# Performance work log

Measured on AMD Instinct MI355X. Metric: run time of the kernel, lower is better.

## Reference

```python
import jax, jax.numpy as jnp
import numpy as np

N, K, D = 16384, 16, 16
TWO_PI = 2.0 * np.pi


def setup_inputs() -> dict:
    key = jax.random.key(0)
    k1, k2, k3, k4 = jax.random.split(key, 4)
    X = jax.random.normal(k1, (N, D), dtype=jnp.float32)
    mu = jax.random.normal(k2, (K, D), dtype=jnp.float32)
    L = jax.random.normal(k3, (K, D, D), dtype=jnp.float32)
    weights = jax.random.uniform(k4, (K,), dtype=jnp.float32)
    return {"X": X, "mu": mu, "L": L, "weights": weights, "it": 0}


def reference(X, mu, L, weights, it):
    # Covariance matrices A_k = tril(L_k) @ tril(L_k)^T + I  -> [K, D, D]
    Tl = jnp.tril(L)
    A = jnp.einsum('kab,kcb->kac', Tl, Tl) + jnp.eye(D, dtype=L.dtype)
    Sigma = jnp.linalg.inv(A)                                  # [K, D, D]

    # Gaussian product for all pairs (i, j):
    #   S_ij = inv(Sigma_i + Sigma_j), m_ij = S_ij (Sigma_i mu_i + Sigma_j mu_j)
    Ssum = Sigma[:, None] + Sigma[None, :]                     # [K, K, D, D]
    S = jnp.linalg.inv(Ssum)                                   # [K, K, D, D]
    rhs = jnp.einsum('kab,kb->ka', Sigma, mu)                  # Sigma_k mu_k
    m = jnp.einsum('ijab,ijb->ija', S, rhs[:, None] + rhs[None, :])  # [K, K, D]

    # Normalizer of the product Gaussian: z_ij = ((2pi)^D det(S_ij))^(-1/2)
    z = 1.0 / jnp.sqrt((TWO_PI ** D) * jnp.linalg.det(S))      # [K, K]
    P = jnp.linalg.inv(S)                                      # precision, [K, K, D, D]

    # Pair coefficient _product_z(i, j) (uses A as covariance here, as in source)
    Asum = A[:, None] + A[None, :]                             # [K, K, D, D]
    dmu = mu[:, None] - mu[None, :]                            # [K, K, D]
    q_mu = jnp.einsum('ijd,ijde,ije->ij', dmu, jnp.linalg.inv(Asum), dmu)
    pz = jnp.exp(-0.5 * q_mu) / jnp.sqrt(jnp.linalg.det(TWO_PI * Asum))

    # Mahalanobis distance of every sample to every pair mean: [N, K, K]
    diff = X[:, None, None, :] - m[None]                       # [N, K, K, D]
    quad = jnp.einsum('nijd,ijde,nije->nij', diff, P, diff)

    coef = pz * z * (weights[:, None] * weights[None, :])      # [K, K]
    pdf = jnp.einsum('ij,nij->n', coef, jnp.exp(-0.5 * quad))  # [N]
    return jnp.mean(jnp.log(pdf))
```

## Files before the change

### kernel.cpp

```cpp
#include <hip/hip_runtime.h>
#include <math.h>

#define NTOT 16384
#define KK 16
#define DD 16
#define NPAIR 136

#define NPREP 9

#define WS_RHS   0
#define WS_WP    1024
#define WS_LCS   9792
#define WS_PART  10336
#define WS_END   18528

#define LN2PI 1.8378770664093454836f

#define SROW 17
#define SMAT (SROW * DD)

__device__ __forceinline__ float chol16_rl(float* Mr, int r, float* dinvv) {
  float ld = 0.0f;
  #pragma unroll
  for (int c = 0; c < DD; c++) {
    float d2 = __shfl(Mr[c], c, 16);
    ld += __logf(d2);
    float dinv = rsqrtf(d2);
    dinvv[c] = dinv;
    float v = Mr[c] * dinv;
    Mr[c] = v;
    #pragma unroll
    for (int c2 = c + 1; c2 < DD; c2++)
      Mr[c2] = fmaf(-v, __shfl(v, c2, 16), Mr[c2]);
  }
  return ld;
}

__device__ __forceinline__ float solve16(const float* G, int r,
                                         const float* dinvv, float b) {
  float acc = b, qq = 0.0f;
  #pragma unroll
  for (int m = 0; m < DD; m++) {
    float ym = __shfl(acc, m, 16) * dinvv[m];
    qq = fmaf(ym, ym, qq);
    if (r > m) acc = fmaf(-G[m], ym, acc);
  }
  return qq;
}

__global__ __launch_bounds__(256) void gm_prep(const float* __restrict__ mu,
                                               const float* __restrict__ L,
                                               const float* __restrict__ wts,
                                               char* __restrict__ wsb) {
  __shared__ float sSig[KK * SMAT];
  __shared__ float sA[KK * SMAT];
  __shared__ float sR[256];

  const int tid = threadIdx.x;
  const int k = tid >> 4;
  const int r = tid & 15;

  const float* Lk = L + k * DD * DD;
  float Lx[DD];
  #pragma unroll
  for (int b = 0; b < DD; b++) Lx[b] = (b <= r) ? Lk[r * DD + b] : 0.0f;

  float Ar[DD];
  #pragma unroll
  for (int c = 0; c < DD; c++) {
    float s = (r == c) ? 1.0f : 0.0f;
    #pragma unroll
    for (int b = 0; b <= c; b++)
      s = fmaf(Lx[b], __shfl(Lx[b], c, 16), s);
    Ar[c] = s;
    sA[k * SMAT + r * SROW + c] = s;
  }

  float dinvv[DD];
  chol16_rl(Ar, r, dinvv);

  float Wc[DD];
  {
    float acc[DD];
    #pragma unroll
    for (int m = 0; m < DD; m++) acc[m] = (r == m) ? 1.0f : 0.0f;
    #pragma unroll
    for (int m = 0; m < DD; m++) {
      float w = acc[m] * dinvv[m];
      Wc[m] = w;
      #pragma unroll
      for (int rr = m + 1; rr < DD; rr++)
        acc[rr] = fmaf(-__shfl(Ar[m], rr, 16), w, acc[rr]);
    }
  }
  if (blockIdx.x == 0) {
    float* Wout = (float*)(wsb + WS_WP) + k * 137;
    #pragma unroll
    for (int rr = 0; rr < DD; rr++)
      if (rr >= r) Wout[rr * (rr + 1) / 2 + r] = Wc[rr];
  }

  float Sig[DD];
  #pragma unroll
  for (int b = 0; b < DD; b++) {
    float s = 0.0f;
    #pragma unroll
    for (int rr = 0; rr < DD; rr++)
      s = fmaf(Wc[rr], __shfl(Wc[rr], b, 16), s);
    Sig[b] = s;
    sSig[k * SMAT + r * SROW + b] = s;
  }

  {
    float muv = mu[k * DD + r];
    float s = 0.0f;
    #pragma unroll
    for (int b = 0; b < DD; b++)
      s = fmaf(Sig[b], __shfl(muv, b, 16), s);
    sR[k * DD + r] = s;
    if (blockIdx.x == 0) ((float*)(wsb + WS_RHS))[k * DD + r] = s;
  }
  __syncthreads();

  const int p = blockIdx.x * 16 + k;
  if (p >= NPAIR) return;
  int i = 0, rem = p;
  while (rem >= (KK - i)) { rem -= (KK - i); i++; }
  const int j = i + rem;

  float Mr[DD];
  float dv[DD];

  #pragma unroll
  for (int c = 0; c < DD; c++)
    Mr[c] = sSig[i * SMAT + r * SROW + c] + sSig[j * SMAT + r * SROW + c];
  float ldS = chol16_rl(Mr, r, dv);
  float cq = solve16(Mr, r, dv, sR[i * DD + r] + sR[j * DD + r]);

  #pragma unroll
  for (int c = 0; c < DD; c++)
    Mr[c] = sA[i * SMAT + r * SROW + c] + sA[j * SMAT + r * SROW + c];
  float ldA = chol16_rl(Mr, r, dv);
  float q = solve16(Mr, r, dv, mu[i * DD + r] - mu[j * DD + r]);

  if (r == 0) {
    float lC = -0.5f * q - 0.5f * ldA + 0.5f * ldS - (float)DD * LN2PI
               + __logf(wts[i]) + __logf(wts[j]) - 0.5f * cq;
    if (i < j) lC += 0.69314718056f;
    ((float*)(wsb + WS_LCS))[p] = lC;
  }
}

__global__ __launch_bounds__(256) void gm_main(const float* __restrict__ X,
                                               char* __restrict__ wsb) {
  __shared__ float sW[KK * 137];
  __shared__ float sR[KK * 17];
  __shared__ float sLC[NPAIR];
  __shared__ unsigned char sIJ[NPAIR];
  __shared__ float sX[256];
  __shared__ float sE[16 * 17];
  __shared__ double sD[16];

  const int tid = threadIdx.x;
  const int s = tid >> 4;
  const int r = tid & 15;

  {
    const float* Wp = (const float*)(wsb + WS_WP);
    for (int idx = tid; idx < KK * 137; idx += 256) sW[idx] = Wp[idx];
    const float* Rf = (const float*)(wsb + WS_RHS);
    sR[s * 17 + r] = Rf[tid];
    const float* lc = (const float*)(wsb + WS_LCS);
    if (tid < NPAIR) {
      sLC[tid] = lc[tid];
      int i = 0, rem = tid;
      while (rem >= (KK - i)) { rem -= (KK - i); i++; }
      sIJ[tid] = (unsigned char)((i << 4) | (i + rem));
    }
    if (tid < 64)
      ((float4*)sX)[tid] = ((const float4*)(X + (size_t)blockIdx.x * 256))[tid];
  }
  __syncthreads();

  float x[DD];
  {
    float4 b0 = ((const float4*)sX)[s * 4 + 0];
    float4 b1 = ((const float4*)sX)[s * 4 + 1];
    float4 b2 = ((const float4*)sX)[s * 4 + 2];
    float4 b3 = ((const float4*)sX)[s * 4 + 3];
    x[0]=b0.x; x[1]=b0.y; x[2]=b0.z; x[3]=b0.w;
    x[4]=b1.x; x[5]=b1.y; x[6]=b1.z; x[7]=b1.w;
    x[8]=b2.x; x[9]=b2.y; x[10]=b2.z; x[11]=b2.w;
    x[12]=b3.x; x[13]=b3.y; x[14]=b3.z; x[15]=b3.w;
  }

  {
    const float* Wk = &sW[r * 137];
    float g = 0.0f;
    #pragma unroll
    for (int rr = 0; rr < DD; rr++) {
      float y = 0.0f;
      #pragma unroll
      for (int c = 0; c <= rr; c++) y = fmaf(Wk[rr * (rr + 1) / 2 + c], x[c], y);
      g = fmaf(y, y, g);
    }
    float h = 0.0f;
    #pragma unroll
    for (int d = 0; d < DD; d++) h = fmaf(sR[r * 17 + d], x[d], h);
    sE[s * 17 + r] = fmaf(-0.5f, g, h);
  }
  __syncthreads();

  float val[9];
  float T = -3.0e38f;
  #pragma unroll
  for (int t = 0; t < 9; t++) {
    int p = t * 16 + r;
    if (t < 8 || r < 8) {
      int ij = sIJ[p];
      val[t] = sLC[p] + sE[s * 17 + (ij >> 4)] + sE[s * 17 + (ij & 15)];
    } else {
      val[t] = -3.0e38f;
    }
    T = fmaxf(T, val[t]);
  }
  #pragma unroll
  for (int w = 1; w < 16; w <<= 1) T = fmaxf(T, __shfl_xor(T, w, 16));

  float sum = 0.0f;
  #pragma unroll
  for (int t = 0; t < 9; t++) sum += __expf(val[t] - T);
  #pragma unroll
  for (int w = 1; w < 16; w <<= 1) sum += __shfl_xor(sum, w, 16);

  if (r == 0) sD[s] = (double)(T + __logf(sum));
  __syncthreads();
  if (tid == 0) {
    double acc = 0.0;
    #pragma unroll
    for (int m = 0; m < 16; m++) acc += sD[m];
    ((double*)(wsb + WS_PART))[blockIdx.x] = acc;
  }
}

__global__ __launch_bounds__(256) void gm_fin(const double* __restrict__ part,
                                              float* __restrict__ out) {
  int t = threadIdx.x;
  double v = part[t] + part[t + 256] + part[t + 512] + part[t + 768];
  #pragma unroll
  for (int off = 32; off > 0; off >>= 1) v += __shfl_down(v, off);
  __shared__ double r4[4];
  if ((t & 63) == 0) r4[t >> 6] = v;
  __syncthreads();
  if (t == 0) out[0] = (float)((r4[0] + r4[1] + r4[2] + r4[3]) * (1.0 / 16384.0));
}

extern "C" void kernel_launch(void* const* d_in, const int* in_sizes, int n_in,
                              void* d_out, int out_size, void* d_ws, size_t ws_size,
                              hipStream_t stream) {
  const float* X   = (const float*)d_in[0];
  const float* mu  = (const float*)d_in[1];
  const float* L   = (const float*)d_in[2];
  const float* wts = (const float*)d_in[3];
  char* wsb = (char*)d_ws;
  if (ws_size < WS_END) return;

  hipLaunchKernelGGL(gm_prep, dim3(NPREP), dim3(256), 0, stream, mu, L, wts, wsb);
  hipLaunchKernelGGL(gm_main, dim3(NTOT / 16), dim3(256), 0, stream, X, wsb);
  hipLaunchKernelGGL(gm_fin,  dim3(1), dim3(256), 0, stream,
                     (const double*)(wsb + WS_PART), (float*)d_out);
}
```

Measured before the change: 32.09 us.

## Fuse final reduction into main kernel via fixed-point atomics and interleave dual Cholesky

The separate final-reduction kernel is removed. Each main block now adds its partial log-sum to a global 64-bit fixed-point accumulator with an atomic, and the last block to finish, found through an atomic counter, writes the mean. A memset clears the accumulator and counter before the prep kernel. Separately, the two pairwise Cholesky factorisations and solves in the prep kernel are interleaved to expose more instruction-level parallelism. The gain is one fewer kernel launch and a shorter prep critical path, at the cost of an extra memset launch and fixed-point rounding of the partial sums.

Result: slower. 57.65 us (+79.6%).

```diff
diff --git a/kernel.cpp b/kernel.cpp
--- a/kernel.cpp
+++ b/kernel.cpp
@@ -7,17 +7,62 @@
 #define NPAIR 136
 
 #define NPREP 9
+#define NMAIN 1024
 
 #define WS_RHS   0
 #define WS_WP    1024
 #define WS_LCS   9792
-#define WS_PART  10336
-#define WS_END   18528
+#define WS_ACC   10336
+#define WS_CNT   10344
+#define WS_END   10352
 
 #define LN2PI 1.8378770664093454836f
+#define FXSCALE 268435456.0
 
 #define SROW 17
 #define SMAT (SROW * DD)
+
+__device__ __forceinline__ void chol16_rl2(float* Ms, float* Ma, int r,
+                                           float* dinvS, float* dinvA,
+                                           float& ldS, float& ldA) {
+  float ls = 0.0f, la = 0.0f;
+  #pragma unroll
+  for (int c = 0; c < DD; c++) {
+    float d2s = __shfl(Ms[c], c, 16);
+    float d2a = __shfl(Ma[c], c, 16);
+    ls += __logf(d2s);
+    la += __logf(d2a);
+    float dis = rsqrtf(d2s), dia = rsqrtf(d2a);
+    dinvS[c] = dis; dinvA[c] = dia;
+    float vs = Ms[c] * dis, va = Ma[c] * dia;
+    Ms[c] = vs; Ma[c] = va;
+    #pragma unroll
+    for (int c2 = c + 1; c2 < DD; c2++) {
+      Ms[c2] = fmaf(-vs, __shfl(vs, c2, 16), Ms[c2]);
+      Ma[c2] = fmaf(-va, __shfl(va, c2, 16), Ma[c2]);
+    }
+  }
+  ldS = ls; ldA = la;
+}
+
+__device__ __forceinline__ void solve16_2(const float* Gs, const float* Ga, int r,
+                                          const float* dinvS, const float* dinvA,
+                                          float bs, float ba,
+                                          float& qs, float& qa) {
+  float accS = bs, accA = ba, s = 0.0f, a = 0.0f;
+  #pragma unroll
+  for (int m = 0; m < DD; m++) {
+    float ys = __shfl(accS, m, 16) * dinvS[m];
+    float ya = __shfl(accA, m, 16) * dinvA[m];
+    s = fmaf(ys, ys, s);
+    a = fmaf(ya, ya, a);
+    if (r > m) {
+      accS = fmaf(-Gs[m], ys, accS);
+      accA = fmaf(-Ga[m], ya, accA);
+    }
+  }
+  qs = s; qa = a;
+}
 
 __device__ __forceinline__ float chol16_rl(float* Mr, int r, float* dinvv) {
   float ld = 0.0f;
@@ -36,22 +81,10 @@
   return ld;
 }
 
-__device__ __forceinline__ float solve16(const float* G, int r,
-                                         const float* dinvv, float b) {
-  float acc = b, qq = 0.0f;
-  #pragma unroll
-  for (int m = 0; m < DD; m++) {
-    float ym = __shfl(acc, m, 16) * dinvv[m];
-    qq = fmaf(ym, ym, qq);
-    if (r > m) acc = fmaf(-G[m], ym, acc);
-  }
-  return qq;
-}
-
-__global__ __launch_bounds__(256) void gm_prep(const float* __restrict__ mu,
-                                               const float* __restrict__ L,
-                                               const float* __restrict__ wts,
-                                               char* __restrict__ wsb) {
+__global__ __launch_bounds__(256, 1) void gm_prep(const float* __restrict__ mu,
+                                                  const float* __restrict__ L,
+                                                  const float* __restrict__ wts,
+                                                  char* __restrict__ wsb) {
   __shared__ float sSig[KK * SMAT];
   __shared__ float sA[KK * SMAT];
   __shared__ float sR[256];
@@ -128,20 +161,19 @@
   while (rem >= (KK - i)) { rem -= (KK - i); i++; }
   const int j = i + rem;
 
-  float Mr[DD];
-  float dv[DD];
-
-  #pragma unroll
-  for (int c = 0; c < DD; c++)
-    Mr[c] = sSig[i * SMAT + r * SROW + c] + sSig[j * SMAT + r * SROW + c];
-  float ldS = chol16_rl(Mr, r, dv);
-  float cq = solve16(Mr, r, dv, sR[i * DD + r] + sR[j * DD + r]);
-
-  #pragma unroll
-  for (int c = 0; c < DD; c++)
-    Mr[c] = sA[i * SMAT + r * SROW + c] + sA[j * SMAT + r * SROW + c];
-  float ldA = chol16_rl(Mr, r, dv);
-  float q = solve16(Mr, r, dv, mu[i * DD + r] - mu[j * DD + r]);
+  float Ms[DD], Ma[DD], dvS[DD], dvA[DD];
+  #pragma unroll
+  for (int c = 0; c < DD; c++) {
+    Ms[c] = sSig[i * SMAT + r * SROW + c] + sSig[j * SMAT + r * SROW + c];
+    Ma[c] = sA[i * SMAT + r * SROW + c] + sA[j * SMAT + r * SROW + c];
+  }
+  float ldS, ldA;
+  chol16_rl2(Ms, Ma, r, dvS, dvA, ldS, ldA);
+
+  float cq, q;
+  solve16_2(Ms, Ma, r, dvS, dvA,
+            sR[i * DD + r] + sR[j * DD + r],
+            mu[i * DD + r] - mu[j * DD + r], cq, q);
 
   if (r == 0) {
     float lC = -0.5f * q - 0.5f * ldA + 0.5f * ldS - (float)DD * LN2PI
@@ -152,7 +184,8 @@
 }
 
 __global__ __launch_bounds__(256) void gm_main(const float* __restrict__ X,
-                                               char* __restrict__ wsb) {
+                                               char* __restrict__ wsb,
+                                               float* __restrict__ out) {
   __shared__ float sW[KK * 137];
   __shared__ float sR[KK * 17];
   __shared__ float sLC[NPAIR];
@@ -235,24 +268,24 @@
 
   if (r == 0) sD[s] = (double)(T + __logf(sum));
   __syncthreads();
+
   if (tid == 0) {
     double acc = 0.0;
     #pragma unroll
     for (int m = 0; m < 16; m++) acc += sD[m];
-    ((double*)(wsb + WS_PART))[blockIdx.x] = acc;
-  }
-}
-
-__global__ __launch_bounds__(256) void gm_fin(const double* __restrict__ part,
-                                              float* __restrict__ out) {
-  int t = threadIdx.x;
-  double v = part[t] + part[t + 256] + part[t + 512] + part[t + 768];
-  #pragma unroll
-  for (int off = 32; off > 0; off >>= 1) v += __shfl_down(v, off);
-  __shared__ double r4[4];
-  if ((t & 63) == 0) r4[t >> 6] = v;
-  __syncthreads();
-  if (t == 0) out[0] = (float)((r4[0] + r4[1] + r4[2] + r4[3]) * (1.0 / 16384.0));
+    double scaled = acc * FXSCALE;
+    long long fx = (long long)(scaled + (scaled >= 0.0 ? 0.5 : -0.5));
+    unsigned long long* accp = (unsigned long long*)(wsb + WS_ACC);
+    unsigned long long* cntp = (unsigned long long*)(wsb + WS_CNT);
+    atomicAdd(accp, (unsigned long long)fx);
+    __threadfence();
+    unsigned long long old = atomicAdd(cntp, 1ULL);
+    if (old == (unsigned long long)(NMAIN - 1)) {
+      __threadfence();
+      unsigned long long tot = atomicAdd(accp, 0ULL);
+      out[0] = (float)((double)(long long)tot * (1.0 / FXSCALE) * (1.0 / 16384.0));
+    }
+  }
 }
 
 extern "C" void kernel_launch(void* const* d_in, const int* in_sizes, int n_in,
@@ -265,8 +298,8 @@
   char* wsb = (char*)d_ws;
   if (ws_size < WS_END) return;
 
+  hipMemsetAsync(wsb + WS_ACC, 0, 16, stream);
   hipLaunchKernelGGL(gm_prep, dim3(NPREP), dim3(256), 0, stream, mu, L, wts, wsb);
-  hipLaunchKernelGGL(gm_main, dim3(NTOT / 16), dim3(256), 0, stream, X, wsb);
-  hipLaunchKernelGGL(gm_fin,  dim3(1), dim3(256), 0, stream,
-                     (const double*)(wsb + WS_PART), (float*)d_out);
-}
+  hipLaunchKernelGGL(gm_main, dim3(NMAIN), dim3(256), 0, stream, X, wsb,
+                     (float*)d_out);
+}
```
